# Performance work log

Measured on AMD Instinct MI355X. Metric: run time of the kernel, lower is better.

The kernel has to match this reference:

```python
import math
import jax, jax.numpy as jnp
import numpy as np

IN_CH = 512
OUT_CH = 512
KSIZE = 3
STYLE_DIM = 512
EPS = 1e-8


def setup_inputs() -> dict:
    key = jax.random.key(0)
    ks = jax.random.split(key, 8)
    B, H, W = 16, 32, 32
    x = jax.random.normal(ks[0], (B, IN_CH, H, W), dtype=jnp.float32)
    style = jax.random.normal(ks[1], (B, STYLE_DIM), dtype=jnp.float32)
    noise = jax.random.normal(ks[2], (B, 1, 2 * H, 2 * W), dtype=jnp.float32)
    # learned params (matching torch init semantics)
    conv_weight = jax.random.normal(ks[3], (OUT_CH, IN_CH, KSIZE, KSIZE), dtype=jnp.float32)
    mod_weight = jax.random.normal(ks[4], (IN_CH, STYLE_DIM), dtype=jnp.float32)
    mod_bias = jnp.ones((IN_CH,), dtype=jnp.float32)  # bias_init=1
    noise_weight = jax.random.normal(ks[5], (1,), dtype=jnp.float32) * 0.1
    act_bias = jnp.zeros((OUT_CH,), dtype=jnp.float32)
    return {"x": x, "style": style, "noise": noise, "conv_weight": conv_weight,
            "mod_weight": mod_weight, "mod_bias": mod_bias,
            "noise_weight": noise_weight, "act_bias": act_bias}


def _blur_kernel_2d():
    k = jnp.array([1.0, 3.0, 3.0, 1.0], dtype=jnp.float32)
    k2 = k[None, :] * k[:, None]
    k2 = k2 / k2.sum()
    return k2 * 4.0  # upsample_factor**2


def _styled_conv_up(x, style, conv_weight, mod_weight, mod_bias,
                    noise_weight, act_bias, noise):
    B, C_in, H, W = x.shape
    # EqualLinear modulation: scale = 1/sqrt(style_dim), lr_mul=1
    s = style @ (mod_weight * (1.0 / math.sqrt(STYLE_DIM))).T + mod_bias  # [B, C_in]
    # modulate + demodulate per-sample weights
    wscale = 1.0 / math.sqrt(C_in * KSIZE * KSIZE)
    w = wscale * conv_weight[None] * s[:, None, :, None, None]  # [B, out, in, k, k]
    demod = jax.lax.rsqrt(jnp.sum(w * w, axis=(2, 3, 4)) + EPS)  # [B, out]
    w = w * demod[:, :, None, None, None]
    # conv_transpose2d(stride=2, padding=0) == lhs_dilated conv with spatially
    # flipped kernel. torch passes weight as (in, out, k, k); equivalent OIHW
    # forward kernel is flip(w) with layout (out, in, k, k).
    w_flip = jnp.flip(w, axis=(-2, -1))

    def single(xi, wi):  # xi [in,H,W], wi [out,in,k,k]
        return jax.lax.conv_general_dilated(
            xi[None], wi, window_strides=(1, 1),
            padding=[(KSIZE - 1, KSIZE - 1)] * 2,
            lhs_dilation=(2, 2),
            dimension_numbers=("NCHW", "OIHW", "NCHW"))[0]

    out = jax.vmap(single)(x, w_flip)  # [B, out, 2H+1, 2W+1] for k=3
    # Blur: upfirdn2d(kernel=4x4, pad=(1,1)) -> depthwise valid conv
    Bc, Co, Ho, Wo = out.shape
    kb = _blur_kernel_2d()[None, None]  # [1,1,4,4] (symmetric, flip is a no-op)
    out = jax.lax.conv_general_dilated(
        out.reshape(Bc * Co, 1, Ho, Wo), kb, window_strides=(1, 1),
        padding=[(1, 1), (1, 1)],
        dimension_numbers=("NCHW", "OIHW", "NCHW"))
    out = out.reshape(Bc, Co, Ho + 2 - 3, Wo + 2 - 3)  # [B, out, 2H, 2W]
    # noise injection + FusedLeakyReLU (slope 0.2, scale sqrt(2))
    out = out + noise_weight * noise
    out = jax.nn.leaky_relu(out + act_bias.reshape(1, -1, 1, 1), 0.2) * math.sqrt(2.0)
    return out


def reference(x, style, noise, conv_weight, mod_weight, mod_bias,
              noise_weight, act_bias):
    return _styled_conv_up(x, style, conv_weight, mod_weight, mod_bias,
                           noise_weight, act_bias, noise)
```

## Files before the change

### kernel.cpp

```cpp
#include <hip/hip_runtime.h>
#include <math.h>


typedef __attribute__((ext_vector_type(8))) __bf16 bf16x8;
typedef __attribute__((ext_vector_type(4))) float f32x4;

#define WSCALE 0.014731391274719739f
#define SSCALE 0.044194173824159216f

__device__ __forceinline__ unsigned short f2bf(float f) {
  unsigned u = __builtin_bit_cast(unsigned, f);
  u += 0x7fff + ((u >> 16) & 1);
  return (unsigned short)(u >> 16);
}
__device__ __forceinline__ float bf2f(unsigned short h) {
  unsigned u = ((unsigned)h) << 16;
  return __builtin_bit_cast(float, u);
}

__global__ __launch_bounds__(256) void k_style(
    const float* __restrict__ style, const float* __restrict__ mod_w,
    const float* __restrict__ mod_b, float* __restrict__ s_out) {
  int wid  = (blockIdx.x * 256 + threadIdx.x) >> 6;
  int lane = threadIdx.x & 63;
  int b = wid >> 9, ic = wid & 511;
  float acc = 0.f;
  for (int j = lane; j < 512; j += 64)
    acc += style[b * 512 + j] * mod_w[ic * 512 + j];
  for (int off = 32; off > 0; off >>= 1) acc += __shfl_down(acc, off);
  if (lane == 0) s_out[b * 512 + ic] = acc * SSCALE + mod_b[ic];
}

__global__ __launch_bounds__(256) void k_demod(
    const float* __restrict__ conv_w, const float* __restrict__ s,
    float* __restrict__ dscale) {
  int wid  = (blockIdx.x * 256 + threadIdx.x) >> 6;
  int lane = threadIdx.x & 63;
  int b = wid >> 9, oc = wid & 511;
  float acc = 0.f;
  for (int ic = lane; ic < 512; ic += 64) {
    const float* wp = conv_w + (oc * 512 + ic) * 9;
    float w2 = 0.f;
    #pragma unroll
    for (int k = 0; k < 9; k++) { float w = wp[k]; w2 += w * w; }
    float sv = s[b * 512 + ic];
    acc += sv * sv * w2;
  }
  for (int off = 32; off > 0; off >>= 1) acc += __shfl_down(acc, off);
  if (lane == 0)
    dscale[b * 512 + oc] = WSCALE * rsqrtf(WSCALE * WSCALE * acc + 1e-8f);
}

__global__ __launch_bounds__(256) void k_xs2(
    const float* __restrict__ x, const float* __restrict__ s,
    unsigned short* __restrict__ S2) {
  __shared__ float xt[64][65];
  const int b = blockIdx.z, ic0 = blockIdx.y * 64, r0 = blockIdx.x * 2;
  for (int i = threadIdx.x; i < 4096; i += 256) {
    int icL = i >> 6, pxL = i & 63;
    int gr = r0 + (pxL >> 5), gc = pxL & 31;
    xt[icL][pxL] = x[((b * 512 + ic0 + icL) * 32 + gr) * 32 + gc] * s[b * 512 + ic0 + icL];
  }
  __syncthreads();
  for (int i = threadIdx.x; i < 512; i += 256) {
    int pxL = i >> 3, icO = i & 7;
    unsigned short tmp[8];
    #pragma unroll
    for (int k = 0; k < 8; k++) tmp[k] = f2bf(xt[icO * 8 + k][pxL]);
    int gr = r0 + (pxL >> 5), gc = pxL & 31;
    int R = (gr + 1) * 34 + (gc + 1);
    *(uint4*)(&S2[((size_t)b * 1156 + R) * 512 + ic0 + icO * 8]) = *(const uint4*)tmp;
  }
}

__global__ void k_zero(unsigned short* __restrict__ S2) {
  int b = blockIdx.y, id = blockIdx.x;
  int ry, rx;
  if (id < 34)       { ry = 0;        rx = id; }
  else if (id < 68)  { ry = 33;       rx = id - 34; }
  else if (id < 100) { ry = id - 67;  rx = 0; }
  else               { ry = id - 99;  rx = 33; }
  ((unsigned*)(S2 + ((size_t)b * 1156 + ry * 34 + rx) * 512))[threadIdx.x] = 0;
}

__global__ __launch_bounds__(256) void k_wt(
    const float* __restrict__ conv_w, unsigned short* __restrict__ wt2) {
  int idx = blockIdx.x * 256 + threadIdx.x;
  if (idx >= 9 * 64 * 512 * 8) return;
  int j = idx & 7, oc = (idx >> 3) & 511, icg = (idx >> 12) & 63, t = idx >> 18;
  wt2[idx] = f2bf(conv_w[(oc * 512 + icg * 8 + j) * 9 + t]);
}

__device__ const int TAPN[4]     = {4, 2, 2, 1};
__device__ const int TIDt[4][4]  = {{0,2,6,8},{1,7,0,0},{3,5,0,0},{4,0,0,0}};
__device__ const int TOFFt[4][4] = {{0,-1,-34,-35},{0,-34,0,0},{0,-1,0,0},{0,0,0,0}};

__global__ __launch_bounds__(256, 2) void k_mm2(
    const unsigned short* __restrict__ S2, const unsigned short* __restrict__ wt2,
    const float* __restrict__ dscale, unsigned short* __restrict__ I, int b_base) {
  __shared__ __align__(16) unsigned short A_lds[4][4][128][8];
  __shared__ __align__(16) unsigned short Bs[292][40];

  const int mt = blockIdx.x, nt = blockIdx.y, z = blockIdx.z;
  const int p = z & 3, bl = z >> 2, b = b_base + bl;
  const int oc0 = mt * 128, n0 = nt * 256;
  const int tid = threadIdx.x, lane = tid & 63;
  const int wv = tid >> 6, wm = wv >> 1, wn = wv & 1;
  const int l15 = lane & 15, quad = lane >> 4;
  const int ntap = TAPN[p];

  f32x4 acc[4][8];
  #pragma unroll
  for (int m = 0; m < 4; m++)
    #pragma unroll
    for (int n = 0; n < 8; n++) acc[m][n] = (f32x4)0.f;

  const unsigned short* S2b = S2 + (size_t)b * 1156 * 512;

  for (int ic0 = 0; ic0 < 512; ic0 += 32) {
    __syncthreads();
    for (int i = tid; i < 1168; i += 256) {
      int pxp = i >> 2, icq = i & 3;
      int gpx = n0 - 36 + pxp;
      uint4 v = make_uint4(0u, 0u, 0u, 0u);
      if ((unsigned)gpx < 1156u)
        v = *(const uint4*)(S2b + (size_t)gpx * 512 + ic0 + icq * 8);
      *(uint4*)(&Bs[pxp][icq * 8]) = v;
    }
    for (int i = tid; i < ntap * 512; i += 256) {
      int t = i >> 9, r = i & 511;
      int ocL = r & 127, icq = r >> 7;
      int tg = TIDt[p][t];
      uint4 v = *(const uint4*)(wt2 + (((size_t)(tg * 64) + (ic0 >> 3) + icq) * 512 + oc0 + ocL) * 8);
      *(uint4*)(&A_lds[t][icq][ocL][0]) = v;
    }
    __syncthreads();
    for (int t = 0; t < ntap; t++) {
      const int off = TOFFt[p][t];
      bf16x8 af[4], bfr[8];
      #pragma unroll
      for (int m = 0; m < 4; m++)
        af[m] = *(const bf16x8*)(&A_lds[t][quad][wm * 64 + m * 16 + l15][0]);
      #pragma unroll
      for (int n = 0; n < 8; n++)
        bfr[n] = *(const bf16x8*)(&Bs[36 + wn * 128 + n * 16 + l15 + off][quad * 8]);
      #pragma unroll
      for (int m = 0; m < 4; m++)
        #pragma unroll
        for (int n = 0; n < 8; n++)
          acc[m][n] = __builtin_amdgcn_mfma_f32_16x16x32_bf16(af[m], bfr[n], acc[m][n], 0, 0, 0);
    }
  }

  float dsv[4][4];
  #pragma unroll
  for (int m = 0; m < 4; m++)
    #pragma unroll
    for (int r = 0; r < 4; r++)
      dsv[m][r] = dscale[b * 512 + oc0 + wm * 64 + m * 16 + quad * 4 + r];
  const size_t Ibase = ((size_t)(bl * 4 + p) * 512) * 1096;
  #pragma unroll
  for (int n = 0; n < 8; n++) {
    int nf = n0 + wn * 128 + n * 16 + l15;
    int ry = nf / 34, rx = nf - ry * 34;
    if (ry >= 1 && ry <= 33 && rx >= 1) {
      int ul = (ry - 1) * 33 + (rx - 1);
      #pragma unroll
      for (int m = 0; m < 4; m++) {
        int oc = oc0 + wm * 64 + m * 16 + quad * 4;
        #pragma unroll
        for (int r = 0; r < 4; r++)
          I[Ibase + (size_t)(oc + r) * 1096 + ul] = f2bf(acc[m][n][r] * dsv[m][r]);
      }
    }
  }
}

__global__ __launch_bounds__(256) void k_blur(
    const unsigned short* __restrict__ I, const float* __restrict__ noise,
    const float* __restrict__ noise_w, const float* __restrict__ act_b,
    float* __restrict__ out, int b_base) {
  __shared__ __align__(16) unsigned short Ism[4][1096];
  __shared__ float V[64][67];
  const int oc = blockIdx.x, bl = blockIdx.y, b = b_base + bl;
  for (int i = threadIdx.x; i < 548; i += 256) {
    int p = i / 137, w = i - p * 137;
    *(uint4*)(&Ism[p][w * 8]) =
        *(const uint4*)(I + ((size_t)(bl * 4 + p) * 512 + oc) * 1096 + w * 8);
  }
  __syncthreads();
  for (int i = threadIdx.x; i < 2112; i += 256) {
    int r = i / 66, col = i - r * 66;
    int px_ = (col >= 33), ux = col - 33 * px_;
    float v0 = (r >= 1) ? bf2f(Ism[2 + px_][(r - 1) * 33 + ux]) : 0.f;
    float a_ = bf2f(Ism[px_][r * 33 + ux]);
    float b_ = bf2f(Ism[2 + px_][r * 33 + ux]);
    float c_ = bf2f(Ism[px_][(r + 1) * 33 + ux]);
    float d_ = bf2f(Ism[2 + px_][(r + 1) * 33 + ux]);
    V[2 * r][col]     = 0.25f * v0 + 0.75f * a_ + 0.75f * b_ + 0.25f * c_;
    V[2 * r + 1][col] = 0.25f * a_ + 0.75f * b_ + 0.75f * c_ + 0.25f * d_;
  }
  __syncthreads();
  const float nw = noise_w[0], ab = act_b[oc];
  for (int i = threadIdx.x; i < 2048; i += 256) {
    int qy = i >> 5, rx = i & 31;
    float w0 = (rx >= 1) ? V[qy][33 + rx - 1] : 0.f;
    float a_ = V[qy][rx];
    float b_ = V[qy][33 + rx];
    float c_ = V[qy][rx + 1];
    float d_ = V[qy][33 + rx + 1];
    float o0 = 0.25f * w0 + 0.75f * a_ + 0.75f * b_ + 0.25f * c_;
    float o1 = 0.25f * a_ + 0.75f * b_ + 0.75f * c_ + 0.25f * d_;
    const float2 nv = *(const float2*)(noise + b * 4096 + qy * 64 + 2 * rx);
    o0 += nw * nv.x + ab;  o1 += nw * nv.y + ab;
    o0 = (o0 > 0.f ? o0 : 0.2f * o0) * 1.4142135623730951f;
    o1 = (o1 > 0.f ? o1 : 0.2f * o1) * 1.4142135623730951f;
    float2 ov = make_float2(o0, o1);
    *(float2*)(out + (((size_t)b * 512 + oc) * 64 + qy) * 64 + 2 * rx) = ov;
  }
}

extern "C" void kernel_launch(void* const* d_in, const int* in_sizes, int n_in,
                              void* d_out, int out_size, void* d_ws, size_t ws_size,
                              hipStream_t stream) {
  const float* x       = (const float*)d_in[0];
  const float* style   = (const float*)d_in[1];
  const float* noise   = (const float*)d_in[2];
  const float* conv_w  = (const float*)d_in[3];
  const float* mod_w   = (const float*)d_in[4];
  const float* mod_b   = (const float*)d_in[5];
  const float* noise_w = (const float*)d_in[6];
  const float* act_b   = (const float*)d_in[7];
  float* out = (float*)d_out;

  char* ws = (char*)d_ws;
  float*          s_ws = (float*)ws;
  float*          d_sc = (float*)(ws + 32768);
  unsigned short* S2   = (unsigned short*)(ws + 65536);
  unsigned short* wt2  = (unsigned short*)(ws + 65536 + 18939904);
  unsigned short* I    = (unsigned short*)(ws + 65536 + 18939904 + 4718592);
  const size_t fixed = 65536ull + 18939904ull + 4718592ull;
  const size_t i_full = (size_t)16 * 4 * 512 * 1096 * 2;

  int nb = 16;
  if (ws_size < fixed + i_full)     nb = 8;
  if (ws_size < fixed + i_full / 2) nb = 4;
  if (ws_size < fixed + i_full / 4) nb = 2;

  k_style<<<2048, 256, 0, stream>>>(style, mod_w, mod_b, s_ws);
  k_demod<<<2048, 256, 0, stream>>>(conv_w, s_ws, d_sc);
  k_xs2<<<dim3(16, 8, 16), 256, 0, stream>>>(x, s_ws, S2);
  k_zero<<<dim3(132, 16), 256, 0, stream>>>(S2);
  k_wt<<<9216, 256, 0, stream>>>(conv_w, wt2);
  for (int b0 = 0; b0 < 16; b0 += nb) {
    k_mm2<<<dim3(4, 5, nb * 4), 256, 0, stream>>>(S2, wt2, d_sc, I, b0);
    k_blur<<<dim3(512, nb), 256, 0, stream>>>(I, noise, noise_w, act_b, out, b0);
  }
}
```

Before: 473.7 us.

## Replace phase-split transposed conv GEMM with per-tap GEMM and col2im in blur

Restructures the transposed convolution as one dense GEMM over all 9 taps (M=9*512 taps×out-channels, N=1024 pixels, K=512), writing per-tap outputs T, then scatters/sums taps into the 4 sub-pixel phases inside the blur kernel. This removes padded/halo handling and uneven per-phase tap counts in the GEMM and uses XOR-swizzled LDS with a larger K-step. In exchange the intermediate grows from 4 phase planes to 9 tap planes per batch, raising memory traffic and workspace, and the blur kernel does extra LDS work. It also precomputes squared weight sums once to simplify demodulation.

Result: faster. 402.7 us (-15.0%).

```diff
diff --git a/kernel.cpp b/kernel.cpp
--- a/kernel.cpp
+++ b/kernel.cpp
@@ -31,27 +31,42 @@
   if (lane == 0) s_out[b * 512 + ic] = acc * SSCALE + mod_b[ic];
 }
 
+__global__ __launch_bounds__(256) void k_w2(
+    const float* __restrict__ conv_w, unsigned short* __restrict__ W2,
+    float* __restrict__ w2s) {
+  __shared__ float t[4608];
+  const int oc = blockIdx.x;
+  for (int i = threadIdx.x; i < 4608; i += 256) t[i] = conv_w[oc * 4608 + i];
+  __syncthreads();
+  for (int i = threadIdx.x; i < 4608; i += 256) {
+    int tg = i >> 9, ic = i & 511;
+    W2[((size_t)(tg * 512 + oc)) * 512 + ic] = f2bf(t[ic * 9 + tg]);
+  }
+  for (int i = threadIdx.x; i < 512; i += 256) {
+    float a = 0.f;
+    #pragma unroll
+    for (int tg = 0; tg < 9; tg++) { float w = t[i * 9 + tg]; a += w * w; }
+    w2s[oc * 512 + i] = a;
+  }
+}
+
 __global__ __launch_bounds__(256) void k_demod(
-    const float* __restrict__ conv_w, const float* __restrict__ s,
+    const float* __restrict__ w2s, const float* __restrict__ s,
     float* __restrict__ dscale) {
   int wid  = (blockIdx.x * 256 + threadIdx.x) >> 6;
   int lane = threadIdx.x & 63;
   int b = wid >> 9, oc = wid & 511;
   float acc = 0.f;
   for (int ic = lane; ic < 512; ic += 64) {
-    const float* wp = conv_w + (oc * 512 + ic) * 9;
-    float w2 = 0.f;
-    #pragma unroll
-    for (int k = 0; k < 9; k++) { float w = wp[k]; w2 += w * w; }
     float sv = s[b * 512 + ic];
-    acc += sv * sv * w2;
+    acc += sv * sv * w2s[oc * 512 + ic];
   }
   for (int off = 32; off > 0; off >>= 1) acc += __shfl_down(acc, off);
   if (lane == 0)
     dscale[b * 512 + oc] = WSCALE * rsqrtf(WSCALE * WSCALE * acc + 1e-8f);
 }
 
-__global__ __launch_bounds__(256) void k_xs2(
+__global__ __launch_bounds__(256) void k_xs(
     const float* __restrict__ x, const float* __restrict__ s,
     unsigned short* __restrict__ S2) {
   __shared__ float xt[64][65];
@@ -68,46 +83,27 @@
     #pragma unroll
     for (int k = 0; k < 8; k++) tmp[k] = f2bf(xt[icO * 8 + k][pxL]);
     int gr = r0 + (pxL >> 5), gc = pxL & 31;
-    int R = (gr + 1) * 34 + (gc + 1);
-    *(uint4*)(&S2[((size_t)b * 1156 + R) * 512 + ic0 + icO * 8]) = *(const uint4*)tmp;
-  }
-}
-
-__global__ void k_zero(unsigned short* __restrict__ S2) {
-  int b = blockIdx.y, id = blockIdx.x;
-  int ry, rx;
-  if (id < 34)       { ry = 0;        rx = id; }
-  else if (id < 68)  { ry = 33;       rx = id - 34; }
-  else if (id < 100) { ry = id - 67;  rx = 0; }
-  else               { ry = id - 99;  rx = 33; }
-  ((unsigned*)(S2 + ((size_t)b * 1156 + ry * 34 + rx) * 512))[threadIdx.x] = 0;
-}
-
-__global__ __launch_bounds__(256) void k_wt(
-    const float* __restrict__ conv_w, unsigned short* __restrict__ wt2) {
-  int idx = blockIdx.x * 256 + threadIdx.x;
-  if (idx >= 9 * 64 * 512 * 8) return;
-  int j = idx & 7, oc = (idx >> 3) & 511, icg = (idx >> 12) & 63, t = idx >> 18;
-  wt2[idx] = f2bf(conv_w[(oc * 512 + icg * 8 + j) * 9 + t]);
-}
-
-__device__ const int TAPN[4]     = {4, 2, 2, 1};
-__device__ const int TIDt[4][4]  = {{0,2,6,8},{1,7,0,0},{3,5,0,0},{4,0,0,0}};
-__device__ const int TOFFt[4][4] = {{0,-1,-34,-35},{0,-34,0,0},{0,-1,0,0},{0,0,0,0}};
-
-__global__ __launch_bounds__(256, 2) void k_mm2(
-    const unsigned short* __restrict__ S2, const unsigned short* __restrict__ wt2,
-    const float* __restrict__ dscale, unsigned short* __restrict__ I, int b_base) {
-  __shared__ __align__(16) unsigned short A_lds[4][4][128][8];
-  __shared__ __align__(16) unsigned short Bs[292][40];
-
-  const int mt = blockIdx.x, nt = blockIdx.y, z = blockIdx.z;
-  const int p = z & 3, bl = z >> 2, b = b_base + bl;
-  const int oc0 = mt * 128, n0 = nt * 256;
+    *(uint4*)(&S2[((size_t)b * 1024 + gr * 32 + gc) * 512 + ic0 + icO * 8]) =
+        *(const uint4*)tmp;
+  }
+}
+
+__global__ __launch_bounds__(256, 2) void k_gemm(
+    const unsigned short* __restrict__ S2, const unsigned short* __restrict__ W2,
+    const float* __restrict__ dscale, unsigned short* __restrict__ T, int b_base) {
+  __shared__ __align__(16) unsigned short As[128][64];
+  __shared__ __align__(16) unsigned short Bs[256][64];
+
+  const int mt = blockIdx.x;
+  const int nt = blockIdx.y;
+  const int bl = blockIdx.z, b = b_base + bl;
+  const int m0 = mt * 128;
   const int tid = threadIdx.x, lane = tid & 63;
   const int wv = tid >> 6, wm = wv >> 1, wn = wv & 1;
   const int l15 = lane & 15, quad = lane >> 4;
-  const int ntap = TAPN[p];
+
+  const unsigned short* __restrict__ Ag = W2 + (size_t)m0 * 512;
+  const unsigned short* __restrict__ Bg = S2 + ((size_t)b * 1024 + nt * 256) * 512;
 
   f32x4 acc[4][8];
   #pragma unroll
@@ -115,35 +111,35 @@
     #pragma unroll
     for (int n = 0; n < 8; n++) acc[m][n] = (f32x4)0.f;
 
-  const unsigned short* S2b = S2 + (size_t)b * 1156 * 512;
-
-  for (int ic0 = 0; ic0 < 512; ic0 += 32) {
+  #pragma unroll 1
+  for (int ic0 = 0; ic0 < 512; ic0 += 64) {
     __syncthreads();
-    for (int i = tid; i < 1168; i += 256) {
-      int pxp = i >> 2, icq = i & 3;
-      int gpx = n0 - 36 + pxp;
-      uint4 v = make_uint4(0u, 0u, 0u, 0u);
-      if ((unsigned)gpx < 1156u)
-        v = *(const uint4*)(S2b + (size_t)gpx * 512 + ic0 + icq * 8);
-      *(uint4*)(&Bs[pxp][icq * 8]) = v;
-    }
-    for (int i = tid; i < ntap * 512; i += 256) {
-      int t = i >> 9, r = i & 511;
-      int ocL = r & 127, icq = r >> 7;
-      int tg = TIDt[p][t];
-      uint4 v = *(const uint4*)(wt2 + (((size_t)(tg * 64) + (ic0 >> 3) + icq) * 512 + oc0 + ocL) * 8);
-      *(uint4*)(&A_lds[t][icq][ocL][0]) = v;
+    #pragma unroll
+    for (int it = 0; it < 4; it++) {
+      int c = it * 256 + tid, r = c >> 3, kq = c & 7;
+      uint4 v = *(const uint4*)(Ag + (size_t)r * 512 + ic0 + kq * 8);
+      *(uint4*)(&As[r][(kq ^ (r & 7)) * 8]) = v;
+    }
+    #pragma unroll
+    for (int it = 0; it < 8; it++) {
+      int c = it * 256 + tid, r = c >> 3, kq = c & 7;
+      uint4 v = *(const uint4*)(Bg + (size_t)r * 512 + ic0 + kq * 8);
+      *(uint4*)(&Bs[r][(kq ^ (r & 7)) * 8]) = v;
     }
     __syncthreads();
-    for (int t = 0; t < ntap; t++) {
-      const int off = TOFFt[p][t];
+    #pragma unroll
+    for (int kk = 0; kk < 2; kk++) {
       bf16x8 af[4], bfr[8];
       #pragma unroll
-      for (int m = 0; m < 4; m++)
-        af[m] = *(const bf16x8*)(&A_lds[t][quad][wm * 64 + m * 16 + l15][0]);
-      #pragma unroll
-      for (int n = 0; n < 8; n++)
-        bfr[n] = *(const bf16x8*)(&Bs[36 + wn * 128 + n * 16 + l15 + off][quad * 8]);
+      for (int m = 0; m < 4; m++) {
+        int r = wm * 64 + m * 16 + l15;
+        af[m] = *(const bf16x8*)(&As[r][((kk * 4 + quad) ^ (r & 7)) * 8]);
+      }
+      #pragma unroll
+      for (int n = 0; n < 8; n++) {
+        int r = wn * 128 + n * 16 + l15;
+        bfr[n] = *(const bf16x8*)(&Bs[r][((kk * 4 + quad) ^ (r & 7)) * 8]);
+      }
       #pragma unroll
       for (int m = 0; m < 4; m++)
         #pragma unroll
@@ -152,41 +148,58 @@
     }
   }
 
+  const int t = mt >> 2, ocb = (mt & 3) * 128;
   float dsv[4][4];
   #pragma unroll
   for (int m = 0; m < 4; m++)
     #pragma unroll
     for (int r = 0; r < 4; r++)
-      dsv[m][r] = dscale[b * 512 + oc0 + wm * 64 + m * 16 + quad * 4 + r];
-  const size_t Ibase = ((size_t)(bl * 4 + p) * 512) * 1096;
+      dsv[m][r] = dscale[b * 512 + ocb + wm * 64 + m * 16 + quad * 4 + r];
+  const size_t Tbase = ((size_t)(bl * 9 + t)) * 512 * 1024;
   #pragma unroll
   for (int n = 0; n < 8; n++) {
-    int nf = n0 + wn * 128 + n * 16 + l15;
-    int ry = nf / 34, rx = nf - ry * 34;
-    if (ry >= 1 && ry <= 33 && rx >= 1) {
-      int ul = (ry - 1) * 33 + (rx - 1);
-      #pragma unroll
-      for (int m = 0; m < 4; m++) {
-        int oc = oc0 + wm * 64 + m * 16 + quad * 4;
-        #pragma unroll
-        for (int r = 0; r < 4; r++)
-          I[Ibase + (size_t)(oc + r) * 1096 + ul] = f2bf(acc[m][n][r] * dsv[m][r]);
-      }
+    int px = nt * 256 + wn * 128 + n * 16 + l15;
+    #pragma unroll
+    for (int m = 0; m < 4; m++) {
+      int oc = ocb + wm * 64 + m * 16 + quad * 4;
+      #pragma unroll
+      for (int r = 0; r < 4; r++)
+        T[Tbase + (size_t)(oc + r) * 1024 + px] = f2bf(acc[m][n][r] * dsv[m][r]);
     }
   }
 }
 
 __global__ __launch_bounds__(256) void k_blur(
-    const unsigned short* __restrict__ I, const float* __restrict__ noise,
+    const unsigned short* __restrict__ T, const float* __restrict__ noise,
     const float* __restrict__ noise_w, const float* __restrict__ act_b,
     float* __restrict__ out, int b_base) {
-  __shared__ __align__(16) unsigned short Ism[4][1096];
+  __shared__ __align__(16) unsigned short Tm[9][1024];
+  __shared__ unsigned short Ism[4][1089];
   __shared__ float V[64][67];
   const int oc = blockIdx.x, bl = blockIdx.y, b = b_base + bl;
-  for (int i = threadIdx.x; i < 548; i += 256) {
-    int p = i / 137, w = i - p * 137;
-    *(uint4*)(&Ism[p][w * 8]) =
-        *(const uint4*)(I + ((size_t)(bl * 4 + p) * 512 + oc) * 1096 + w * 8);
+  for (int i = threadIdx.x; i < 1152; i += 256) {
+    int tg = i >> 7, w = i & 127;
+    *(uint4*)(&Tm[tg][w * 8]) =
+        *(const uint4*)(T + ((size_t)(bl * 9 + tg) * 512 + oc) * 1024 + w * 8);
+  }
+  __syncthreads();
+  for (int i = threadIdx.x; i < 4356; i += 256) {
+    int p = i / 1089, u = i - p * 1089;
+    int uy = u / 33, ux = u - uy * 33;
+    int py = p >> 1, pxp = p & 1;
+    float acc = 0.f;
+    int na = py ? 1 : 2, nc = pxp ? 1 : 2;
+    for (int a = 0; a < na; a++) {
+      int ky = py ? 1 : a * 2;
+      int iy = uy - (ky == 2);
+      for (int c = 0; c < nc; c++) {
+        int kx = pxp ? 1 : c * 2;
+        int ix = ux - (kx == 2);
+        if ((unsigned)iy < 32u && (unsigned)ix < 32u)
+          acc += bf2f(Tm[ky * 3 + kx][iy * 32 + ix]);
+      }
+    }
+    Ism[p][u] = f2bf(acc);
   }
   __syncthreads();
   for (int i = threadIdx.x; i < 2112; i += 256) {
@@ -236,24 +249,25 @@
   char* ws = (char*)d_ws;
   float*          s_ws = (float*)ws;
   float*          d_sc = (float*)(ws + 32768);
-  unsigned short* S2   = (unsigned short*)(ws + 65536);
-  unsigned short* wt2  = (unsigned short*)(ws + 65536 + 18939904);
-  unsigned short* I    = (unsigned short*)(ws + 65536 + 18939904 + 4718592);
-  const size_t fixed = 65536ull + 18939904ull + 4718592ull;
-  const size_t i_full = (size_t)16 * 4 * 512 * 1096 * 2;
+  float*          w2s  = (float*)(ws + 65536);
+  unsigned short* S2   = (unsigned short*)(ws + 65536 + 1048576);
+  unsigned short* W2   = (unsigned short*)(ws + 65536 + 1048576 + 16777216);
+  unsigned short* T    = (unsigned short*)(ws + 65536 + 1048576 + 16777216 + 4718592);
+  const size_t fixed  = 65536ull + 1048576ull + 16777216ull + 4718592ull;
+  const size_t t_full = (size_t)16 * 9 * 512 * 1024 * 2;
 
   int nb = 16;
-  if (ws_size < fixed + i_full)     nb = 8;
-  if (ws_size < fixed + i_full / 2) nb = 4;
-  if (ws_size < fixed + i_full / 4) nb = 2;
+  if (ws_size < fixed + t_full)     nb = 8;
+  if (ws_size < fixed + t_full / 2) nb = 4;
+  if (ws_size < fixed + t_full / 4) nb = 2;
+  if (ws_size < fixed + t_full / 8) nb = 1;
 
   k_style<<<2048, 256, 0, stream>>>(style, mod_w, mod_b, s_ws);
-  k_demod<<<2048, 256, 0, stream>>>(conv_w, s_ws, d_sc);
-  k_xs2<<<dim3(16, 8, 16), 256, 0, stream>>>(x, s_ws, S2);
-  k_zero<<<dim3(132, 16), 256, 0, stream>>>(S2);
-  k_wt<<<9216, 256, 0, stream>>>(conv_w, wt2);
+  k_w2<<<512, 256, 0, stream>>>(conv_w, W2, w2s);
+  k_demod<<<2048, 256, 0, stream>>>(w2s, s_ws, d_sc);
+  k_xs<<<dim3(16, 8, 16), 256, 0, stream>>>(x, s_ws, S2);
   for (int b0 = 0; b0 < 16; b0 += nb) {
-    k_mm2<<<dim3(4, 5, nb * 4), 256, 0, stream>>>(S2, wt2, d_sc, I, b0);
-    k_blur<<<dim3(512, nb), 256, 0, stream>>>(I, noise, noise_w, act_b, out, b0);
-  }
-}
+    k_gemm<<<dim3(36, 4, nb), 256, 0, stream>>>(S2, W2, d_sc, T, b0);
+    k_blur<<<dim3(512, nb), 256, 0, stream>>>(T, noise, noise_w, act_b, out, b0);
+  }
+}
```
